# Kernel tuning notes

Hardware: AMD Instinct MI355X
Metric: run time of the kernel (lower is better)

The kernel has to match this reference:

```python
import jax, jax.numpy as jnp
from jax import lax
import numpy as np

B, L, M, D = 128, 1024, 68, 2
H = 256          # lstm hidden
IN = M * D       # 136
FF1, FF2 = 256, 512
NLAYERS = 3


def _p(key, shape, scale=0.05):
    return (jax.random.normal(key, shape, dtype=jnp.float32) * scale)


def setup_inputs() -> dict:
    key = jax.random.key(0)
    ks = jax.random.split(key, 20)
    inp = {
        "x": jax.random.normal(ks[0], (B, L, M, D), dtype=jnp.float32),
        "length": jax.random.randint(ks[1], (B,), 1, L + 1, dtype=jnp.int32),
        # MLP: Linear(136,256) -> ReLU -> Linear(256,512) -> ReLU
        "W1": _p(ks[2], (FF1, IN)), "b1": _p(ks[3], (FF1,)),
        "W2": _p(ks[4], (FF2, FF1)), "b2": _p(ks[5], (FF2,)),
        # 3-layer LSTM(512 -> 256), torch gate order i,f,g,o
        "w_ih0": _p(ks[6], (4 * H, FF2)), "w_hh0": _p(ks[7], (4 * H, H)),
        "b_ih0": _p(ks[8], (4 * H,)), "b_hh0": _p(ks[9], (4 * H,)),
        "w_ih1": _p(ks[10], (4 * H, H)), "w_hh1": _p(ks[11], (4 * H, H)),
        "b_ih1": _p(ks[12], (4 * H,)), "b_hh1": _p(ks[13], (4 * H,)),
        "w_ih2": _p(ks[14], (4 * H, H)), "w_hh2": _p(ks[15], (4 * H, H)),
        "b_ih2": _p(ks[16], (4 * H,)), "b_hh2": _p(ks[17], (4 * H,)),
        # decision head Linear(256, 1)
        "Wd": _p(ks[18], (1, H)), "bd": _p(ks[19], (1,)),
    }
    return inp


def lstm_layer(x, w_ih, w_hh, b_ih, b_hh):
    # x: [B, L, Din] -> [B, L, H]; zero initial (h, c)
    b, l, _ = x.shape
    h = w_hh.shape[1]
    xg = jnp.einsum('bld,gd->blg', x, w_ih) + b_ih + b_hh  # [B,L,4H]
    xg = jnp.swapaxes(xg, 0, 1)  # [L,B,4H]

    def step(carry, xt):
        hh, cc = carry
        gates = xt + hh @ w_hh.T
        i, f, g, o = jnp.split(gates, 4, axis=-1)
        i = jax.nn.sigmoid(i)
        f = jax.nn.sigmoid(f)
        g = jnp.tanh(g)
        o = jax.nn.sigmoid(o)
        cc = f * cc + i * g
        hh = o * jnp.tanh(cc)
        return (hh, cc), hh

    init = (jnp.zeros((b, h), x.dtype), jnp.zeros((b, h), x.dtype))
    _, hs = lax.scan(step, init, xg)
    return jnp.swapaxes(hs, 0, 1)  # [B,L,H]


def reference(x, length, W1, b1, W2, b2,
              w_ih0, w_hh0, b_ih0, b_hh0,
              w_ih1, w_hh1, b_ih1, b_hh1,
              w_ih2, w_hh2, b_ih2, b_hh2,
              Wd, bd):
    b, l, m, d = x.shape
    feat = x.reshape(b, l, m * d)
    feat = jax.nn.relu(jnp.einsum('bld,od->blo', feat, W1) + b1)
    feat = jax.nn.relu(jnp.einsum('bld,od->blo', feat, W2) + b2)  # [B,L,512]
    h = lstm_layer(feat, w_ih0, w_hh0, b_ih0, b_hh0)
    h = lstm_layer(h, w_ih1, w_hh1, b_ih1, b_hh1)
    h = lstm_layer(h, w_ih2, w_hh2, b_ih2, b_hh2)  # [B,L,256]
    decision = jnp.einsum('blh,oh->blo', h, Wd)[..., 0] + bd[0]  # [B,L]
    # ragged mean over the first length[i] timesteps (AdaptiveAvgPool1d(1))
    mask = (jnp.arange(l)[None, :] < length[:, None]).astype(decision.dtype)
    out = jnp.sum(decision * mask, axis=1) / length.astype(decision.dtype)
    return out  # [B]
```

## Files before the change

### kernel.cpp

```cpp
#include <hip/hip_runtime.h>
#include <hip/hip_fp16.h>

#define TCH 256
#define NCH 4

typedef __attribute__((ext_vector_type(8))) _Float16 half8;
typedef __attribute__((ext_vector_type(4))) float floatx4;

__device__ __forceinline__ float sigm(float x) {
  return __builtin_amdgcn_rcpf(1.f + __builtin_amdgcn_exp2f(x * -1.44269504f));
}
__device__ __forceinline__ float tanha(float x) {
  return 1.f - 2.f * __builtin_amdgcn_rcpf(1.f + __builtin_amdgcn_exp2f(x * 2.88539009f));
}

template<bool AF32, bool RELUB>
__global__ __launch_bounds__(256, 2) void gemm_k(
    const void* __restrict__ Ab, const float* __restrict__ Bw,
    const float* __restrict__ bias, __half* __restrict__ C,
    const int* __restrict__ length, int K, int KT, int N, int arst, int t0)
{
  int b = blockIdx.x >> 1;
  int tloc0 = (blockIdx.x & 1) << 7;
  if (t0 + tloc0 >= length[b]) return;

  __shared__ half8 As[128][5];
  __shared__ half8 Bs[128][5];

  int tid = threadIdx.x;
  int wave = tid >> 6, lane = tid & 63;
  int wm = (wave & 1) << 6, wn = (wave >> 1) << 6;
  int quad = lane >> 4, sub = lane & 15;
  int n0 = blockIdx.y << 7;

  floatx4 acc[4][4];
#pragma unroll
  for (int i = 0; i < 4; ++i)
#pragma unroll
    for (int j = 0; j < 4; ++j)
#pragma unroll
      for (int e = 0; e < 4; ++e) acc[i][j][e] = 0.f;

  size_t arowbase = (size_t)b * arst + tloc0;

  for (int kt = 0; kt < KT; ++kt) {
    int k0 = kt << 5;
#pragma unroll
    for (int pass = 0; pass < 2; ++pass) {
      int idx = tid + (pass << 8);
      int r = idx >> 2, c8 = (idx & 3) << 3;
      int kb = k0 + c8;
      half8 v;
      if (AF32) {
        const float* src = (const float*)Ab + (arowbase + r) * K + kb;
        if (kb + 8 <= K) {
          float4 u0 = *(const float4*)(src);
          float4 u1 = *(const float4*)(src + 4);
          v[0] = (_Float16)u0.x; v[1] = (_Float16)u0.y; v[2] = (_Float16)u0.z; v[3] = (_Float16)u0.w;
          v[4] = (_Float16)u1.x; v[5] = (_Float16)u1.y; v[6] = (_Float16)u1.z; v[7] = (_Float16)u1.w;
        } else {
#pragma unroll
          for (int i = 0; i < 8; ++i) v[i] = (kb + i < K) ? (_Float16)src[i] : (_Float16)0.f;
        }
      } else {
        const __half* src = (const __half*)Ab + (arowbase + r) * K + kb;
        if (kb + 8 <= K) v = *(const half8*)src;
        else {
#pragma unroll
          for (int i = 0; i < 8; ++i) v[i] = (kb + i < K) ? *(const _Float16*)(src + i) : (_Float16)0.f;
        }
      }
      As[r][c8 >> 3] = v;
      const float* bsrc = Bw + (size_t)(n0 + r) * K + kb;
      half8 w;
      if (kb + 8 <= K) {
        float4 u0 = *(const float4*)(bsrc);
        float4 u1 = *(const float4*)(bsrc + 4);
        w[0] = (_Float16)u0.x; w[1] = (_Float16)u0.y; w[2] = (_Float16)u0.z; w[3] = (_Float16)u0.w;
        w[4] = (_Float16)u1.x; w[5] = (_Float16)u1.y; w[6] = (_Float16)u1.z; w[7] = (_Float16)u1.w;
      } else {
#pragma unroll
        for (int i = 0; i < 8; ++i) w[i] = (kb + i < K) ? (_Float16)bsrc[i] : (_Float16)0.f;
      }
      Bs[r][c8 >> 3] = w;
    }
    __syncthreads();
    half8 af[4], bfr[4];
#pragma unroll
    for (int i = 0; i < 4; ++i) {
      af[i] = As[wm + (i << 4) + sub][quad];
      bfr[i] = Bs[wn + (i << 4) + sub][quad];
    }
#pragma unroll
    for (int mt = 0; mt < 4; ++mt)
#pragma unroll
      for (int nt = 0; nt < 4; ++nt)
        acc[mt][nt] = __builtin_amdgcn_mfma_f32_16x16x32_f16(af[mt], bfr[nt], acc[mt][nt], 0, 0, 0);
    __syncthreads();
  }
  size_t mrowbase = (size_t)blockIdx.x << 7;
#pragma unroll
  for (int nt = 0; nt < 4; ++nt) {
    int n = n0 + wn + (nt << 4) + sub;
    float bv = 0.f;
    if (RELUB) bv = bias[n];
#pragma unroll
    for (int mt = 0; mt < 4; ++mt) {
#pragma unroll
      for (int r4 = 0; r4 < 4; ++r4) {
        int m = wm + (mt << 4) + (quad << 2) + r4;
        float v = acc[mt][nt][r4] + bv;
        if (RELUB) v = fmaxf(v, 0.f);
        C[(mrowbase + m) * (size_t)N + n] = __float2half(v);
      }
    }
  }
}

__global__ void pack_whh(const float* __restrict__ whh, __half* __restrict__ wpk)
{
  int idx = blockIdx.x;
  int lane = threadIdx.x;
  int kc = idx & 7, gt = (idx >> 3) & 3, w = (idx >> 5) & 7, hf = idx >> 8;
  int n = (gt << 8) + (hf << 7) + (w << 4) + (lane & 15);
  int k = (kc << 5) + ((lane >> 4) << 3);
  const float* src = whh + (size_t)n * 256 + k;
  half8 v;
#pragma unroll
  for (int e = 0; e < 8; ++e) v[e] = (_Float16)src[e];
  ((half8*)wpk)[((size_t)idx << 6) + lane] = v;
}

__global__ __launch_bounds__(512, 2) void scan_mf(
    const __half* __restrict__ xg, const __half* __restrict__ wpk,
    const float* __restrict__ bih, const float* __restrict__ bhh,
    __half* __restrict__ hout, __half* __restrict__ hsave,
    float* __restrict__ csave, unsigned long long* __restrict__ exch,
    const int* __restrict__ length, int t0)
{
  int bid = blockIdx.x;
  int g = bid & 7, hf = bid >> 3;
  int sid = (g << 1) | hf;
  int tid = threadIdx.x;
  int w = tid >> 6, lane = tid & 63;
  int q = lane >> 4, r = lane & 15;

  int maxlen = 0;
#pragma unroll
  for (int i = 0; i < 16; ++i) maxlen = max(maxlen, length[(g << 4) + i]);
  int tend = min(t0 + TCH, maxlen);
  if (t0 >= tend) return;

  __shared__ __align__(16) unsigned short hfr[4096];

  half8 bf[4][8];
  {
    const half8* wpb = (const half8*)wpk;
#pragma unroll
    for (int gt = 0; gt < 4; ++gt)
#pragma unroll
      for (int s = 0; s < 8; ++s) {
        int kc = (s < 4) ? ((hf << 2) + s) : (((1 - hf) << 2) + (s - 4));
        int fi = ((((hf << 3) + w) << 2) + gt) * 8 + kc;
        bf[gt][s] = wpb[((size_t)fi << 6) + lane];
      }
  }

  int nbase = (hf << 7) + (w << 4) + r;
  float bsum[4];
#pragma unroll
  for (int gt = 0; gt < 4; ++gt) bsum[gt] = bih[(gt << 8) + nbase] + bhh[(gt << 8) + nbase];

  const __half* xb[4];
#pragma unroll
  for (int rr = 0; rr < 4; ++rr)
    xb[rr] = xg + ((size_t)((g << 4) + (q << 2) + rr) * TCH) * 1024 + nbase;

  float c0[4];
  if (t0 == 0) {
    ((uint4*)hfr)[tid] = uint4{0, 0, 0, 0};
#pragma unroll
    for (int rr = 0; rr < 4; ++rr) c0[rr] = 0.f;
  } else {
    if (tid < 256)
      ((uint4*)hfr)[tid] = ((const uint4*)(hsave + ((size_t)sid << 11)))[tid];
    else
      ((uint4*)hfr)[tid] = ((const uint4*)(hsave + ((size_t)(sid ^ 1) << 11)))[tid - 256];
    int i = (w << 4) + r;
#pragma unroll
    for (int rr = 0; rr < 4; ++rr)
      c0[rr] = csave[((size_t)sid << 11) + (i << 4) + (q << 2) + rr];
  }
  __syncthreads();

  unsigned long long* exA = exch + ((size_t)sid << 11);
  const unsigned long long* exB = exch + ((size_t)(sid ^ 1) << 11);

  unsigned* h1w = (unsigned*)hfr;
  unsigned* h2w = (unsigned*)(hfr + 2048);
  int widx0 = tid << 1;
  int m_c = widx0 >> 6, p0 = widx0 & 63;
  unsigned cuoff = ((unsigned)(p0 >> 4) << 8) + ((unsigned)((p0 >> 2) & 3) << 6)
                 + ((unsigned)m_c << 2) + (unsigned)(p0 & 3);

  unsigned long long pw[2];

  for (int t = t0; t < tend; ++t) {
    int tl = t - t0;
    half8 afo[4];
#pragma unroll
    for (int s = 0; s < 4; ++s)
      afo[s] = *(const half8*)&hfr[((s << 6) + lane) << 3];

    __half xh[4][4];
#pragma unroll
    for (int gt = 0; gt < 4; ++gt)
#pragma unroll
      for (int rr = 0; rr < 4; ++rr)
        xh[gt][rr] = xb[rr][((size_t)tl << 10) + (gt << 8)];

    floatx4 acc[4];
#pragma unroll
    for (int gt = 0; gt < 4; ++gt)
#pragma unroll
      for (int e = 0; e < 4; ++e) acc[gt][e] = bsum[gt];

#pragma unroll
    for (int s = 0; s < 4; ++s)
#pragma unroll
      for (int gt = 0; gt < 4; ++gt)
        acc[gt] = __builtin_amdgcn_mfma_f32_16x16x32_f16(afo[s], bf[gt][s], acc[gt], 0, 0, 0);

    if (tl > 0) {
      const unsigned long long* pb = exB + ((size_t)(t & 1) << 10) + widx0;
      int guard = 0;
      for (;;) {
        bool ok = ((int)(unsigned)(pw[0] >> 32) == t) &&
                  ((int)(unsigned)(pw[1] >> 32) == t);
        if (ok || ++guard > (1 << 20)) break;
        __builtin_amdgcn_s_sleep(1);
        pw[0] = __hip_atomic_load(pb, __ATOMIC_RELAXED, __HIP_MEMORY_SCOPE_AGENT);
        pw[1] = __hip_atomic_load(pb + 1, __ATOMIC_RELAXED, __HIP_MEMORY_SCOPE_AGENT);
      }
      *(uint2*)&h2w[cuoff] = uint2{(unsigned)pw[0], (unsigned)pw[1]};
    }
    __syncthreads();

    half8 afp[4];
#pragma unroll
    for (int s = 0; s < 4; ++s)
      afp[s] = *(const half8*)&hfr[2048 + (((s << 6) + lane) << 3)];
#pragma unroll
    for (int s = 0; s < 4; ++s)
#pragma unroll
      for (int gt = 0; gt < 4; ++gt)
        acc[gt] = __builtin_amdgcn_mfma_f32_16x16x32_f16(afp[s], bf[gt][4 + s], acc[gt], 0, 0, 0);

    unsigned prv[4];
#pragma unroll
    for (int rr = 0; rr < 4; ++rr) {
      float iv = sigm(acc[0][rr] + __half2float(xh[0][rr]));
      float fv = sigm(acc[1][rr] + __half2float(xh[1][rr]));
      float gv = tanha(acc[2][rr] + __half2float(xh[2][rr]));
      float ov = sigm(acc[3][rr] + __half2float(xh[3][rr]));
      float c = fmaf(fv, c0[rr], iv * gv);
      c0[rr] = c;
      float hv = ov * tanha(c);
      __half hh = __float2half(hv);
      int m = (q << 2) + rr;
      hout[((size_t)(((g << 4) + m) * TCH + tl) << 8) + nbase] = hh;
      unsigned hu = (unsigned)__half_as_ushort(hh);
      unsigned ot = (unsigned)__shfl_xor((int)hu, 1);
      prv[rr] = (ot << 16) | hu;
    }
    if (!(r & 1)) {
      unsigned long long tg = ((unsigned long long)(unsigned)(t + 1)) << 32;
      unsigned long long* dstb = exA + ((size_t)((t + 1) & 1) << 10);
#pragma unroll
      for (int rr = 0; rr < 4; ++rr) {
        int m = (q << 2) + rr;
        h1w[((w >> 1) << 8) + ((((w & 1) << 1) | (r >> 3)) << 6) + (m << 2) + ((r & 7) >> 1)] = prv[rr];
        int widx = (m << 6) + (w << 3) + (r >> 1);
        __hip_atomic_store(dstb + widx, tg | (unsigned long long)prv[rr],
                           __ATOMIC_RELAXED, __HIP_MEMORY_SCOPE_AGENT);
      }
    }
    if (t + 1 < tend) {
      const unsigned long long* pb = exB + ((size_t)((t + 1) & 1) << 10) + widx0;
      pw[0] = __hip_atomic_load(pb, __ATOMIC_RELAXED, __HIP_MEMORY_SCOPE_AGENT);
      pw[1] = __hip_atomic_load(pb + 1, __ATOMIC_RELAXED, __HIP_MEMORY_SCOPE_AGENT);
    }
    __syncthreads();
  }

  if (tid < 256)
    ((uint4*)(hsave + ((size_t)sid << 11)))[tid] = ((const uint4*)hfr)[tid];
  {
    int i = (w << 4) + r;
#pragma unroll
    for (int rr = 0; rr < 4; ++rr)
      csave[((size_t)sid << 11) + (i << 4) + (q << 2) + rr] = c0[rr];
  }
}

__global__ __launch_bounds__(256, 2) void head_k(
    const __half* __restrict__ h2, const float* __restrict__ Wd,
    const float* __restrict__ bd, const int* __restrict__ length,
    float* __restrict__ dacc, float* __restrict__ out, int t0, int first, int last)
{
  int b = blockIdx.x, tid = threadIdx.x;
  int lane = tid & 63, wave = tid >> 6;
  int len = length[b];
  int tend = min(t0 + TCH, len);
  float4 w4 = *(const float4*)(Wd + (lane << 2));
  float wsum = 0.f;
  for (int t = t0 + wave; t < tend; t += 4) {
    const __half* hr = h2 + (((size_t)b * TCH) + (t - t0)) * 256 + (lane << 2);
    uint2 u = *(const uint2*)hr;
    __half2 p0 = __builtin_bit_cast(__half2, u.x);
    __half2 p1 = __builtin_bit_cast(__half2, u.y);
    float s = w4.x * __half2float(p0.x) + w4.y * __half2float(p0.y)
            + w4.z * __half2float(p1.x) + w4.w * __half2float(p1.y);
#pragma unroll
    for (int off = 32; off > 0; off >>= 1) s += __shfl_xor(s, off);
    wsum += s;
  }
  __shared__ float wred[4];
  if (lane == 0) wred[wave] = wsum;
  __syncthreads();
  if (tid == 0) {
    int cnt = tend - t0; if (cnt < 0) cnt = 0;
    float tot = wred[0] + wred[1] + wred[2] + wred[3] + bd[0] * (float)cnt;
    if (!first) tot += dacc[b];
    dacc[b] = tot;
    if (last) out[b] = tot / (float)len;
  }
}

extern "C" void kernel_launch(void* const* d_in, const int* in_sizes, int n_in,
                              void* d_out, int out_size, void* d_ws, size_t ws_size,
                              hipStream_t stream) {
  (void)in_sizes; (void)n_in; (void)out_size; (void)ws_size;
  const float* x    = (const float*)d_in[0];
  const int* length = (const int*)d_in[1];
  const float* W1   = (const float*)d_in[2];
  const float* b1   = (const float*)d_in[3];
  const float* W2   = (const float*)d_in[4];
  const float* b2   = (const float*)d_in[5];
  const float* wih[3] = {(const float*)d_in[6],  (const float*)d_in[10], (const float*)d_in[14]};
  const float* whh[3] = {(const float*)d_in[7],  (const float*)d_in[11], (const float*)d_in[15]};
  const float* bih[3] = {(const float*)d_in[8],  (const float*)d_in[12], (const float*)d_in[16]};
  const float* bhh[3] = {(const float*)d_in[9],  (const float*)d_in[13], (const float*)d_in[17]};
  const float* Wd   = (const float*)d_in[18];
  const float* bd   = (const float*)d_in[19];
  float* out = (float*)d_out;

  char* ws = (char*)d_ws;
  __half* XG    = (__half*)(ws);
  __half* FEAT2 = (__half*)(ws + 67108864);
  __half* FEAT1 = (__half*)(ws + 100663296);
  __half* HBUF  = FEAT1;
  __half* WPK   = (__half*)(ws + 117440512);
  __half* HSV   = (__half*)(ws + 119013376);
  float*  CSV   = (float*)(ws + 119209984);
  unsigned long long* EXC = (unsigned long long*)(ws + 119603200);
  float* DACC   = (float*)(ws + 120389632);

  for (int l = 0; l < 3; ++l)
    pack_whh<<<512, 64, 0, stream>>>(whh[l], WPK + (size_t)l * 262144);

  for (int c = 0; c < NCH; ++c) {
    int t0 = c * TCH;
    gemm_k<true,  true ><<<dim3(256, 2), 256, 0, stream>>>(
        (const void*)(x + (size_t)t0 * 136), W1, b1, FEAT1, length, 136, 5, 256, 1024, t0);
    gemm_k<false, true ><<<dim3(256, 4), 256, 0, stream>>>(
        (const void*)FEAT1, W2, b2, FEAT2, length, 256, 8, 512, TCH, t0);
    gemm_k<false, false><<<dim3(256, 8), 256, 0, stream>>>(
        (const void*)FEAT2, wih[0], nullptr, XG, length, 512, 16, 1024, TCH, t0);
    scan_mf<<<16, 512, 0, stream>>>(XG, WPK, bih[0], bhh[0], HBUF,
                                    HSV, CSV, EXC, length, t0);
    gemm_k<false, false><<<dim3(256, 8), 256, 0, stream>>>(
        (const void*)HBUF, wih[1], nullptr, XG, length, 256, 8, 1024, TCH, t0);
    scan_mf<<<16, 512, 0, stream>>>(XG, WPK + 262144, bih[1], bhh[1], HBUF,
                                    HSV + 32768, CSV + 32768, EXC + 32768, length, t0);
    gemm_k<false, false><<<dim3(256, 8), 256, 0, stream>>>(
        (const void*)HBUF, wih[2], nullptr, XG, length, 256, 8, 1024, TCH, t0);
    scan_mf<<<16, 512, 0, stream>>>(XG, WPK + 524288, bih[2], bhh[2], HBUF,
                                    HSV + 65536, CSV + 65536, EXC + 65536, length, t0);
    head_k<<<128, 256, 0, stream>>>(HBUF, Wd, bd, length, DACC, out, t0, c == 0, c == NCH - 1);
  }
}
```

Before: 7.729 ms.

## Split LSTM scan hidden dimension across four blocks per batch group

The recurrent scan now splits each 16-sequence group's 256 hidden units across four 256-thread blocks instead of two 512-thread blocks, giving 32 workgroups. Each block computes 64 hidden units and, at every timestep, gathers the other three quarters of h through flag-tagged atomic exchange slots in global memory. The aim is to spread the serial recurrence over more compute units and shorten each block's per-step MFMA and activation work. In exchange, every step now waits on three peers instead of one, which adds polling and cross-block latency.

Measured after the change: 8.366 ms. 1.08x slower.

```diff
diff --git a/kernel.cpp b/kernel.cpp
--- a/kernel.cpp
+++ b/kernel.cpp
@@ -121,8 +121,8 @@
 {
   int idx = blockIdx.x;
   int lane = threadIdx.x;
-  int kc = idx & 7, gt = (idx >> 3) & 3, w = (idx >> 5) & 7, hf = idx >> 8;
-  int n = (gt << 8) + (hf << 7) + (w << 4) + (lane & 15);
+  int kc = idx & 7, gt = (idx >> 3) & 3, w = (idx >> 5) & 3, qd = (idx >> 7) & 3;
+  int n = (gt << 8) + (qd << 6) + (w << 4) + (lane & 15);
   int k = (kc << 5) + ((lane >> 4) << 3);
   const float* src = whh + (size_t)n * 256 + k;
   half8 v;
@@ -131,7 +131,7 @@
   ((half8*)wpk)[((size_t)idx << 6) + lane] = v;
 }
 
-__global__ __launch_bounds__(512, 2) void scan_mf(
+__global__ __launch_bounds__(256, 1) void scan_mf(
     const __half* __restrict__ xg, const __half* __restrict__ wpk,
     const float* __restrict__ bih, const float* __restrict__ bhh,
     __half* __restrict__ hout, __half* __restrict__ hsave,
@@ -139,8 +139,8 @@
     const int* __restrict__ length, int t0)
 {
   int bid = blockIdx.x;
-  int g = bid & 7, hf = bid >> 3;
-  int sid = (g << 1) | hf;
+  int g = bid & 7, qd = bid >> 3;
+  int sid = (g << 2) + qd;
   int tid = threadIdx.x;
   int w = tid >> 6, lane = tid & 63;
   int q = lane >> 4, r = lane & 15;
@@ -153,63 +153,77 @@
 
   __shared__ __align__(16) unsigned short hfr[4096];
 
+  int sp[3];
+#pragma unroll
+  for (int pi = 0; pi < 3; ++pi) sp[pi] = (g << 2) + ((qd + 1 + pi) & 3);
+
   half8 bf[4][8];
   {
     const half8* wpb = (const half8*)wpk;
 #pragma unroll
     for (int gt = 0; gt < 4; ++gt)
 #pragma unroll
-      for (int s = 0; s < 8; ++s) {
-        int kc = (s < 4) ? ((hf << 2) + s) : (((1 - hf) << 2) + (s - 4));
-        int fi = ((((hf << 3) + w) << 2) + gt) * 8 + kc;
-        bf[gt][s] = wpb[((size_t)fi << 6) + lane];
-      }
-  }
-
-  int nbase = (hf << 7) + (w << 4) + r;
+      for (int j = 0; j < 8; ++j) {
+        int kc = (((qd + (j >> 1)) & 3) << 1) + (j & 1);
+        int fi = ((((qd << 2) + w) << 2) + gt) * 8 + kc;
+        bf[gt][j] = wpb[((size_t)fi << 6) + lane];
+      }
+  }
+
+  int hbase = (qd << 6) + (w << 4) + r;
   float bsum[4];
 #pragma unroll
-  for (int gt = 0; gt < 4; ++gt) bsum[gt] = bih[(gt << 8) + nbase] + bhh[(gt << 8) + nbase];
+  for (int gt = 0; gt < 4; ++gt) bsum[gt] = bih[(gt << 8) + hbase] + bhh[(gt << 8) + hbase];
 
   const __half* xb[4];
 #pragma unroll
   for (int rr = 0; rr < 4; ++rr)
-    xb[rr] = xg + ((size_t)((g << 4) + (q << 2) + rr) * TCH) * 1024 + nbase;
+    xb[rr] = xg + ((size_t)((g << 4) + (q << 2) + rr) * TCH) * 1024 + hbase;
 
   float c0[4];
   if (t0 == 0) {
     ((uint4*)hfr)[tid] = uint4{0, 0, 0, 0};
+    ((uint4*)hfr)[256 + tid] = uint4{0, 0, 0, 0};
 #pragma unroll
     for (int rr = 0; rr < 4; ++rr) c0[rr] = 0.f;
   } else {
-    if (tid < 256)
-      ((uint4*)hfr)[tid] = ((const uint4*)(hsave + ((size_t)sid << 11)))[tid];
-    else
-      ((uint4*)hfr)[tid] = ((const uint4*)(hsave + ((size_t)(sid ^ 1) << 11)))[tid - 256];
+#pragma unroll
+    for (int ii = 0; ii < 2; ++ii) {
+      int idx = tid + (ii << 8);
+      uint4 v;
+      if (idx < 128) {
+        v = ((const uint4*)(hsave + ((size_t)sid << 10)))[idx];
+      } else {
+        int ri = (idx - 128) >> 7, wd = (idx - 128) & 127;
+        v = ((const uint4*)(hsave + ((size_t)sp[ri] << 10)))[wd];
+      }
+      ((uint4*)hfr)[idx] = v;
+    }
     int i = (w << 4) + r;
 #pragma unroll
     for (int rr = 0; rr < 4; ++rr)
-      c0[rr] = csave[((size_t)sid << 11) + (i << 4) + (q << 2) + rr];
+      c0[rr] = csave[((size_t)sid << 10) + (i << 4) + (q << 2) + rr];
   }
   __syncthreads();
 
-  unsigned long long* exA = exch + ((size_t)sid << 11);
-  const unsigned long long* exB = exch + ((size_t)(sid ^ 1) << 11);
+  unsigned long long* exA = exch + ((size_t)sid << 10);
+  const unsigned long long* exB[3];
+#pragma unroll
+  for (int pi = 0; pi < 3; ++pi) exB[pi] = exch + ((size_t)sp[pi] << 10);
 
   unsigned* h1w = (unsigned*)hfr;
-  unsigned* h2w = (unsigned*)(hfr + 2048);
   int widx0 = tid << 1;
-  int m_c = widx0 >> 6, p0 = widx0 & 63;
-  unsigned cuoff = ((unsigned)(p0 >> 4) << 8) + ((unsigned)((p0 >> 2) & 3) << 6)
-                 + ((unsigned)m_c << 2) + (unsigned)(p0 & 3);
-
-  unsigned long long pw[2];
+  int m_c = widx0 >> 5, p0 = widx0 & 31;
+  unsigned cuoff = ((unsigned)(p0 >> 4) << 8) | ((unsigned)((p0 >> 2) & 3) << 6)
+                 | ((unsigned)m_c << 2) | (unsigned)(p0 & 3);
+
+  unsigned long long pw[6];
 
   for (int t = t0; t < tend; ++t) {
     int tl = t - t0;
-    half8 afo[4];
-#pragma unroll
-    for (int s = 0; s < 4; ++s)
+    half8 afo[2];
+#pragma unroll
+    for (int s = 0; s < 2; ++s)
       afo[s] = *(const half8*)&hfr[((s << 6) + lane) << 3];
 
     __half xh[4][4];
@@ -226,35 +240,43 @@
       for (int e = 0; e < 4; ++e) acc[gt][e] = bsum[gt];
 
 #pragma unroll
-    for (int s = 0; s < 4; ++s)
+    for (int s = 0; s < 2; ++s)
 #pragma unroll
       for (int gt = 0; gt < 4; ++gt)
         acc[gt] = __builtin_amdgcn_mfma_f32_16x16x32_f16(afo[s], bf[gt][s], acc[gt], 0, 0, 0);
 
     if (tl > 0) {
-      const unsigned long long* pb = exB + ((size_t)(t & 1) << 10) + widx0;
       int guard = 0;
       for (;;) {
-        bool ok = ((int)(unsigned)(pw[0] >> 32) == t) &&
-                  ((int)(unsigned)(pw[1] >> 32) == t);
+        bool ok = true;
+#pragma unroll
+        for (int j = 0; j < 6; ++j)
+          if ((int)(unsigned)(pw[j] >> 32) != t) ok = false;
         if (ok || ++guard > (1 << 20)) break;
         __builtin_amdgcn_s_sleep(1);
-        pw[0] = __hip_atomic_load(pb, __ATOMIC_RELAXED, __HIP_MEMORY_SCOPE_AGENT);
-        pw[1] = __hip_atomic_load(pb + 1, __ATOMIC_RELAXED, __HIP_MEMORY_SCOPE_AGENT);
-      }
-      *(uint2*)&h2w[cuoff] = uint2{(unsigned)pw[0], (unsigned)pw[1]};
+#pragma unroll
+        for (int ri = 0; ri < 3; ++ri) {
+          const unsigned long long* pb = exB[ri] + ((size_t)(t & 1) << 9) + widx0;
+          pw[(ri << 1)] = __hip_atomic_load(pb, __ATOMIC_RELAXED, __HIP_MEMORY_SCOPE_AGENT);
+          pw[(ri << 1) + 1] = __hip_atomic_load(pb + 1, __ATOMIC_RELAXED, __HIP_MEMORY_SCOPE_AGENT);
+        }
+      }
+#pragma unroll
+      for (int ri = 0; ri < 3; ++ri)
+        *(uint2*)&h1w[((1 + ri) << 9) + cuoff] =
+            uint2{(unsigned)pw[(ri << 1)], (unsigned)pw[(ri << 1) + 1]};
     }
     __syncthreads();
 
-    half8 afp[4];
-#pragma unroll
-    for (int s = 0; s < 4; ++s)
-      afp[s] = *(const half8*)&hfr[2048 + (((s << 6) + lane) << 3)];
-#pragma unroll
-    for (int s = 0; s < 4; ++s)
+    half8 afp[6];
+#pragma unroll
+    for (int s = 0; s < 6; ++s)
+      afp[s] = *(const half8*)&hfr[(((2 + s) << 6) + lane) << 3];
+#pragma unroll
+    for (int s = 0; s < 6; ++s)
 #pragma unroll
       for (int gt = 0; gt < 4; ++gt)
-        acc[gt] = __builtin_amdgcn_mfma_f32_16x16x32_f16(afp[s], bf[gt][4 + s], acc[gt], 0, 0, 0);
+        acc[gt] = __builtin_amdgcn_mfma_f32_16x16x32_f16(afp[s], bf[gt][2 + s], acc[gt], 0, 0, 0);
 
     unsigned prv[4];
 #pragma unroll
@@ -268,38 +290,41 @@
       float hv = ov * tanha(c);
       __half hh = __float2half(hv);
       int m = (q << 2) + rr;
-      hout[((size_t)(((g << 4) + m) * TCH + tl) << 8) + nbase] = hh;
+      hout[((size_t)(((g << 4) + m) * TCH + tl) << 8) + hbase] = hh;
       unsigned hu = (unsigned)__half_as_ushort(hh);
       unsigned ot = (unsigned)__shfl_xor((int)hu, 1);
       prv[rr] = (ot << 16) | hu;
     }
     if (!(r & 1)) {
       unsigned long long tg = ((unsigned long long)(unsigned)(t + 1)) << 32;
-      unsigned long long* dstb = exA + ((size_t)((t + 1) & 1) << 10);
+      unsigned long long* dstb = exA + ((size_t)((t + 1) & 1) << 9);
 #pragma unroll
       for (int rr = 0; rr < 4; ++rr) {
         int m = (q << 2) + rr;
         h1w[((w >> 1) << 8) + ((((w & 1) << 1) | (r >> 3)) << 6) + (m << 2) + ((r & 7) >> 1)] = prv[rr];
-        int widx = (m << 6) + (w << 3) + (r >> 1);
+        int widx = (m << 5) + (w << 3) + (r >> 1);
         __hip_atomic_store(dstb + widx, tg | (unsigned long long)prv[rr],
                            __ATOMIC_RELAXED, __HIP_MEMORY_SCOPE_AGENT);
       }
     }
     if (t + 1 < tend) {
-      const unsigned long long* pb = exB + ((size_t)((t + 1) & 1) << 10) + widx0;
-      pw[0] = __hip_atomic_load(pb, __ATOMIC_RELAXED, __HIP_MEMORY_SCOPE_AGENT);
-      pw[1] = __hip_atomic_load(pb + 1, __ATOMIC_RELAXED, __HIP_MEMORY_SCOPE_AGENT);
+#pragma unroll
+      for (int ri = 0; ri < 3; ++ri) {
+        const unsigned long long* pb = exB[ri] + ((size_t)((t + 1) & 1) << 9) + widx0;
+        pw[(ri << 1)] = __hip_atomic_load(pb, __ATOMIC_RELAXED, __HIP_MEMORY_SCOPE_AGENT);
+        pw[(ri << 1) + 1] = __hip_atomic_load(pb + 1, __ATOMIC_RELAXED, __HIP_MEMORY_SCOPE_AGENT);
+      }
     }
     __syncthreads();
   }
 
-  if (tid < 256)
-    ((uint4*)(hsave + ((size_t)sid << 11)))[tid] = ((const uint4*)hfr)[tid];
+  if (tid < 128)
+    ((uint4*)(hsave + ((size_t)sid << 10)))[tid] = ((const uint4*)hfr)[tid];
   {
     int i = (w << 4) + r;
 #pragma unroll
     for (int rr = 0; rr < 4; ++rr)
-      csave[((size_t)sid << 11) + (i << 4) + (q << 2) + rr] = c0[rr];
+      csave[((size_t)sid << 10) + (i << 4) + (q << 2) + rr] = c0[rr];
   }
 }
 
@@ -377,15 +402,15 @@
         (const void*)FEAT1, W2, b2, FEAT2, length, 256, 8, 512, TCH, t0);
     gemm_k<false, false><<<dim3(256, 8), 256, 0, stream>>>(
         (const void*)FEAT2, wih[0], nullptr, XG, length, 512, 16, 1024, TCH, t0);
-    scan_mf<<<16, 512, 0, stream>>>(XG, WPK, bih[0], bhh[0], HBUF,
+    scan_mf<<<32, 256, 0, stream>>>(XG, WPK, bih[0], bhh[0], HBUF,
                                     HSV, CSV, EXC, length, t0);
     gemm_k<false, false><<<dim3(256, 8), 256, 0, stream>>>(
         (const void*)HBUF, wih[1], nullptr, XG, length, 256, 8, 1024, TCH, t0);
-    scan_mf<<<16, 512, 0, stream>>>(XG, WPK + 262144, bih[1], bhh[1], HBUF,
+    scan_mf<<<32, 256, 0, stream>>>(XG, WPK + 262144, bih[1], bhh[1], HBUF,
                                     HSV + 32768, CSV + 32768, EXC + 32768, length, t0);
     gemm_k<false, false><<<dim3(256, 8), 256, 0, stream>>>(
         (const void*)HBUF, wih[2], nullptr, XG, length, 256, 8, 1024, TCH, t0);
-    scan_mf<<<16, 512, 0, stream>>>(XG, WPK + 524288, bih[2], bhh[2], HBUF,
+    scan_mf<<<32, 256, 0, stream>>>(XG, WPK + 524288, bih[2], bhh[2], HBUF,
                                     HSV + 65536, CSV + 65536, EXC + 65536, length, t0);
     head_k<<<128, 256, 0, stream>>>(HBUF, Wd, bd, length, DACC, out, t0, c == 0, c == NCH - 1);
   }
```
